# Optimization experiments

Hardware: AMD Instinct MI355X
Metric: run time of the kernel (lower is better)

Reference implementation:

```python
import jax, jax.numpy as jnp
import numpy as np

N = 50000      # nodes
E = 800000     # directed edges (before self-loops)
F_IN = 128     # input features
HID = 64       # hidden channels per head (conv1)
HEADS = 4      # attention heads (conv1)
C = 47         # num classes (conv2 out, 1 output head, concat=False)
NEG_SLOPE = 0.2


def _glorot(key, shape):
    fan = shape[0] + shape[-1] if len(shape) > 1 else shape[-1]
    lim = float(np.sqrt(6.0 / fan))
    return jax.random.uniform(key, shape, jnp.float32, -lim, lim)


def setup_inputs() -> dict:
    key = jax.random.key(0)
    ks = jax.random.split(key, 10)
    x = jax.random.normal(ks[0], (N, F_IN), jnp.float32)
    edge_index = jax.random.randint(ks[1], (2, E), 0, N, jnp.int32)
    W1 = _glorot(ks[2], (F_IN, HEADS * HID))
    a_src1 = _glorot(ks[3], (HEADS, HID))
    a_dst1 = _glorot(ks[4], (HEADS, HID))
    b1 = jnp.zeros((HEADS * HID,), jnp.float32)
    W2 = _glorot(ks[5], (HEADS * HID, 1 * C))
    a_src2 = _glorot(ks[6], (1, C))
    a_dst2 = _glorot(ks[7], (1, C))
    b2 = jnp.zeros((C,), jnp.float32)
    return {"x": x, "edge_index": edge_index, "W1": W1, "a_src1": a_src1,
            "a_dst1": a_dst1, "b1": b1, "W2": W2, "a_src2": a_src2,
            "a_dst2": a_dst2, "b2": b2}


def _gat_conv(x, W, a_src, a_dst, b, src, dst, n, heads, out_ch, concat):
    # linear transform, split heads: [n, heads, out_ch]
    h = (x @ W).reshape(n, heads, out_ch)
    # per-node attention logits
    al_s = jnp.sum(h * a_src, axis=-1)            # [n, heads]
    al_d = jnp.sum(h * a_dst, axis=-1)            # [n, heads]
    # per-edge scores (messages flow src -> dst)
    e = jax.nn.leaky_relu(al_s[src] + al_d[dst], NEG_SLOPE)  # [E', heads]
    # scatter-softmax over edges sharing a destination node
    e_max = jax.ops.segment_max(e, dst, num_segments=n)      # [n, heads]
    ex = jnp.exp(e - e_max[dst])
    denom = jax.ops.segment_sum(ex, dst, num_segments=n)
    alpha = ex / (denom[dst] + 1e-16)                        # [E', heads]
    # attention-weighted scatter-add aggregation
    out = jax.ops.segment_sum(h[src] * alpha[:, :, None], dst, num_segments=n)
    out = out.reshape(n, heads * out_ch) if concat else jnp.mean(out, axis=1)
    return out + b


def reference(x, edge_index, W1, a_src1, a_dst1, b1, W2, a_src2, a_dst2, b2):
    n = x.shape[0]
    # add self-loops (PyG GATConv default)
    loops = jnp.arange(n, dtype=edge_index.dtype)
    src = jnp.concatenate([edge_index[0], loops])
    dst = jnp.concatenate([edge_index[1], loops])
    # dropout omitted (eval mode)
    h = jax.nn.elu(_gat_conv(x, W1, a_src1, a_dst1, b1, src, dst, n, HEADS, HID, True))
    out = _gat_conv(h, W2, a_src2, a_dst2, b2, src, dst, n, 1, C, False)
    return jax.nn.log_softmax(out, axis=1)
```

## Files before the change

### kernel.cpp

```cpp
#include <hip/hip_runtime.h>
#include <hip/hip_fp16.h>
#include <math.h>

#define N_NODES 50000
#define E_EDGES 800000
#define E_TOT   850000
#define F_IN    128
#define C1      256
#define NCLS    47
#define H2S     48
#define NEG     0.2f
#define SCAN_B  196

typedef _Float16 f16x8 __attribute__((ext_vector_type(8)));
typedef float    f32x4 __attribute__((ext_vector_type(4)));


__global__ void k_count(const int* __restrict__ ei, int* __restrict__ deg) {
    int i = blockIdx.x * 256 + threadIdx.x;
    if (i >= E_TOT) return;
    int dst = (i < E_EDGES) ? ei[E_EDGES + i] : (i - E_EDGES);
    atomicAdd(&deg[dst], 1);
}

__global__ void k_scan_blk(const int* __restrict__ deg, int* __restrict__ blksum) {
    __shared__ int ws[4];
    int i = blockIdx.x * 256 + threadIdx.x;
    int v = (i < N_NODES) ? deg[i] : 0;
    int lane = threadIdx.x & 63, w = threadIdx.x >> 6;
    #pragma unroll
    for (int off = 32; off; off >>= 1) v += __shfl_xor(v, off);
    if (lane == 0) ws[w] = v;
    __syncthreads();
    if (threadIdx.x == 0) blksum[blockIdx.x] = ws[0] + ws[1] + ws[2] + ws[3];
}

__global__ void k_scan_top(const int* __restrict__ blksum, int* __restrict__ blkoff) {
    __shared__ int ws[4];
    int tid = threadIdx.x, lane = tid & 63, w = tid >> 6;
    int v = (tid < SCAN_B) ? blksum[tid] : 0;
    int sc = v;
    #pragma unroll
    for (int off = 1; off < 64; off <<= 1) {
        int t = __shfl_up(sc, off);
        if (lane >= off) sc += t;
    }
    if (lane == 63) ws[w] = sc;
    __syncthreads();
    if (tid == 0) { int a = 0; for (int t = 0; t < 4; t++) { int u = ws[t]; ws[t] = a; a += u; } }
    __syncthreads();
    if (tid < SCAN_B) blkoff[tid] = sc + ws[w] - v;
}

__global__ void k_scan_fin(const int* __restrict__ deg, const int* __restrict__ blkoff,
                           int* __restrict__ row_ptr, int* __restrict__ cursor) {
    __shared__ int ws[4];
    int i = blockIdx.x * 256 + threadIdx.x;
    int v = (i < N_NODES) ? deg[i] : 0;
    int lane = threadIdx.x & 63, w = threadIdx.x >> 6;
    int sc = v;
    #pragma unroll
    for (int off = 1; off < 64; off <<= 1) {
        int t = __shfl_up(sc, off);
        if (lane >= off) sc += t;
    }
    if (lane == 63) ws[w] = sc;
    __syncthreads();
    if (threadIdx.x == 0) { int a = 0; for (int t = 0; t < 4; t++) { int u = ws[t]; ws[t] = a; a += u; } }
    __syncthreads();
    int incl = sc + ws[w] + blkoff[blockIdx.x];
    if (i < N_NODES) {
        row_ptr[i + 1] = incl;
        cursor[i]      = incl - v;
    }
    if (i == 0) row_ptr[0] = 0;
}

__global__ void k_scatter(const int* __restrict__ ei, int* __restrict__ cursor,
                          int* __restrict__ csr_src) {
    int i = blockIdx.x * 256 + threadIdx.x;
    if (i >= E_TOT) return;
    int src, dst;
    if (i < E_EDGES) { src = ei[i]; dst = ei[E_EDGES + i]; }
    else             { src = dst = i - E_EDGES; }
    int pos = atomicAdd(&cursor[dst], 1);
    csr_src[pos] = src;
}


__global__ void k_prepw2f(const float* __restrict__ W2, uint4* __restrict__ W2f) {
    int t = blockIdx.x * 256 + threadIdx.x;
    if (t >= 1536) return;
    int f = t >> 9, ks = (t >> 6) & 7, lane = t & 63;
    int c  = f * 16 + (lane & 15);
    int kb = ks * 32 + ((lane >> 4) << 3);
    unsigned short h[8];
    #pragma unroll
    for (int j = 0; j < 8; j++) {
        float v = (c < NCLS) ? W2[(size_t)(kb + j) * NCLS + c] : 0.f;
        h[j] = __half_as_ushort(__float2half_rn(v));
    }
    W2f[t] = make_uint4((unsigned)h[0] | ((unsigned)h[1] << 16),
                        (unsigned)h[2] | ((unsigned)h[3] << 16),
                        (unsigned)h[4] | ((unsigned)h[5] << 16),
                        (unsigned)h[6] | ((unsigned)h[7] << 16));
}


__global__ void __launch_bounds__(64)
k_gemm1(const float* __restrict__ x, const float* __restrict__ W1,
        const float* __restrict__ a_src1, const float* __restrict__ a_dst1,
        __half* __restrict__ H1h, float* __restrict__ al_s, float* __restrict__ al_d) {
    __shared__ float xs[16][F_IN];
    int n0 = blockIdx.x * 16;
    int lane = threadIdx.x;
    {
        const float4* xg = (const float4*)(x + (size_t)n0 * F_IN);
        float4* xs4 = (float4*)&xs[0][0];
        #pragma unroll
        for (int j = 0; j < 8; j++) xs4[lane + 64 * j] = xg[lane + 64 * j];
    }
    __syncthreads();
    int c4 = lane * 4;
    float acc[16][4] = {};
    for (int kg = 0; kg < F_IN; kg += 4) {
        float4 w0 = *(const float4*)(W1 + (size_t)(kg + 0) * C1 + c4);
        float4 w1 = *(const float4*)(W1 + (size_t)(kg + 1) * C1 + c4);
        float4 w2 = *(const float4*)(W1 + (size_t)(kg + 2) * C1 + c4);
        float4 w3 = *(const float4*)(W1 + (size_t)(kg + 3) * C1 + c4);
        #pragma unroll
        for (int r = 0; r < 16; r++) {
            float4 xv = *(const float4*)&xs[r][kg];
            acc[r][0] += xv.x * w0.x + xv.y * w1.x + xv.z * w2.x + xv.w * w3.x;
            acc[r][1] += xv.x * w0.y + xv.y * w1.y + xv.z * w2.y + xv.w * w3.y;
            acc[r][2] += xv.x * w0.z + xv.y * w1.z + xv.z * w2.z + xv.w * w3.z;
            acc[r][3] += xv.x * w0.w + xv.y * w1.w + xv.z * w2.w + xv.w * w3.w;
        }
    }
    int h = lane >> 4;
    int cc4 = (lane & 15) * 4;
    float4 as = *(const float4*)(a_src1 + h * 64 + cc4);
    float4 ad = *(const float4*)(a_dst1 + h * 64 + cc4);
    #pragma unroll
    for (int r = 0; r < 16; r++) {
        int n = n0 + r;
        ushort4 pk;
        pk.x = __half_as_ushort(__float2half_rn(acc[r][0]));
        pk.y = __half_as_ushort(__float2half_rn(acc[r][1]));
        pk.z = __half_as_ushort(__float2half_rn(acc[r][2]));
        pk.w = __half_as_ushort(__float2half_rn(acc[r][3]));
        *(ushort4*)(H1h + (size_t)n * C1 + c4) = pk;
        float vs = acc[r][0]*as.x + acc[r][1]*as.y + acc[r][2]*as.z + acc[r][3]*as.w;
        float vd = acc[r][0]*ad.x + acc[r][1]*ad.y + acc[r][2]*ad.z + acc[r][3]*ad.w;
        #pragma unroll
        for (int off = 8; off; off >>= 1) {
            vs += __shfl_xor(vs, off);
            vd += __shfl_xor(vd, off);
        }
        if ((lane & 15) == 0) {
            al_s[n * 4 + h] = vs;
            al_d[n * 4 + h] = vd;
        }
    }
}


__global__ void k_agg1(const __half* __restrict__ H1h, const float* __restrict__ al_s,
                       const float* __restrict__ al_d, const int* __restrict__ row_ptr,
                       const int* __restrict__ csr_src, const float* __restrict__ b1,
                       __half* __restrict__ HEh) {
    int n = blockIdx.x * 4 + (threadIdx.x >> 6);
    int lane = threadIdx.x & 63;
    int h = lane >> 4;
    int beg = row_ptr[n], end = row_ptr[n + 1];
    float ald = al_d[n * 4 + h];
    float m = -INFINITY, s = 0.f;
    float a0 = 0.f, a1 = 0.f, a2 = 0.f, a3 = 0.f;
    int j = beg;
    for (; j + 3 < end; j += 4) {
        int ss[4]; float ee[4]; ushort4 hh[4];
        #pragma unroll
        for (int t = 0; t < 4; t++) ss[t] = csr_src[j + t];
        #pragma unroll
        for (int t = 0; t < 4; t++) ee[t] = al_s[ss[t] * 4 + h];
        #pragma unroll
        for (int t = 0; t < 4; t++)
            hh[t] = *(const ushort4*)(H1h + (size_t)ss[t] * C1 + lane * 4);
        #pragma unroll
        for (int t = 0; t < 4; t++) {
            float e = ee[t] + ald;
            ee[t] = (e >= 0.f) ? e : NEG * e;
        }
        float nm = fmaxf(m, fmaxf(fmaxf(ee[0], ee[1]), fmaxf(ee[2], ee[3])));
        float f = __expf(m - nm);
        m = nm;
        float p[4];
        #pragma unroll
        for (int t = 0; t < 4; t++) p[t] = __expf(ee[t] - nm);
        s = s * f + p[0] + p[1] + p[2] + p[3];
        a0 *= f; a1 *= f; a2 *= f; a3 *= f;
        #pragma unroll
        for (int t = 0; t < 4; t++) {
            a0 += p[t] * __half2float(__ushort_as_half(hh[t].x));
            a1 += p[t] * __half2float(__ushort_as_half(hh[t].y));
            a2 += p[t] * __half2float(__ushort_as_half(hh[t].z));
            a3 += p[t] * __half2float(__ushort_as_half(hh[t].w));
        }
    }
    for (; j < end; j++) {
        int s0 = csr_src[j];
        float e = al_s[s0 * 4 + h] + ald;
        e = (e >= 0.f) ? e : NEG * e;
        ushort4 hv = *(const ushort4*)(H1h + (size_t)s0 * C1 + lane * 4);
        float nm = fmaxf(m, e);
        float f  = __expf(m - nm);
        float pr = __expf(e - nm);
        s  = s  * f + pr;
        a0 = a0 * f + pr * __half2float(__ushort_as_half(hv.x));
        a1 = a1 * f + pr * __half2float(__ushort_as_half(hv.y));
        a2 = a2 * f + pr * __half2float(__ushort_as_half(hv.z));
        a3 = a3 * f + pr * __half2float(__ushort_as_half(hv.w));
        m = nm;
    }
    float inv = 1.f / (s + 1e-16f);
    float4 bb = *(const float4*)(b1 + lane * 4);
    float o0 = a0 * inv + bb.x, o1 = a1 * inv + bb.y;
    float o2 = a2 * inv + bb.z, o3 = a3 * inv + bb.w;
    o0 = (o0 > 0.f) ? o0 : expm1f(o0);
    o1 = (o1 > 0.f) ? o1 : expm1f(o1);
    o2 = (o2 > 0.f) ? o2 : expm1f(o2);
    o3 = (o3 > 0.f) ? o3 : expm1f(o3);
    ushort4 pk;
    pk.x = __half_as_ushort(__float2half_rn(o0));
    pk.y = __half_as_ushort(__float2half_rn(o1));
    pk.z = __half_as_ushort(__float2half_rn(o2));
    pk.w = __half_as_ushort(__float2half_rn(o3));
    *(ushort4*)(HEh + (size_t)n * C1 + lane * 4) = pk;
}


__global__ void __launch_bounds__(64)
k_gemm2(const __half* __restrict__ HEh, const uint4* __restrict__ W2f,
        const float* __restrict__ a_src2, const float* __restrict__ a_dst2,
        __half* __restrict__ H2h, float* __restrict__ al_s2, float* __restrict__ al_d2) {
    int lane = threadIdx.x;
    int n0 = blockIdx.x * 16;
    const __half* aptr = HEh + (size_t)(n0 + (lane & 15)) * C1 + ((lane >> 4) << 3);
    const f16x8* bptr = (const f16x8*)W2f;
    f32x4 acc0 = {0.f, 0.f, 0.f, 0.f};
    f32x4 acc1 = {0.f, 0.f, 0.f, 0.f};
    f32x4 acc2 = {0.f, 0.f, 0.f, 0.f};
    #pragma unroll
    for (int ks = 0; ks < 8; ks++) {
        f16x8 a  = *(const f16x8*)(aptr + ks * 32);
        f16x8 b0 = bptr[(0 * 8 + ks) * 64 + lane];
        f16x8 b1 = bptr[(1 * 8 + ks) * 64 + lane];
        f16x8 b2 = bptr[(2 * 8 + ks) * 64 + lane];
        acc0 = __builtin_amdgcn_mfma_f32_16x16x32_f16(a, b0, acc0, 0, 0, 0);
        acc1 = __builtin_amdgcn_mfma_f32_16x16x32_f16(a, b1, acc1, 0, 0, 0);
        acc2 = __builtin_amdgcn_mfma_f32_16x16x32_f16(a, b2, acc2, 0, 0, 0);
    }
    int col = lane & 15;
    int g4  = (lane >> 4) * 4;
    float as[3], ad[3];
    #pragma unroll
    for (int f = 0; f < 3; f++) {
        int c = f * 16 + col;
        as[f] = (c < NCLS) ? a_src2[c] : 0.f;
        ad[f] = (c < NCLS) ? a_dst2[c] : 0.f;
    }
    #pragma unroll
    for (int reg = 0; reg < 4; reg++) {
        int n = n0 + g4 + reg;
        float v0 = acc0[reg], v1 = acc1[reg], v2 = acc2[reg];
        __half* orow = H2h + (size_t)n * H2S;
        orow[col]      = __float2half_rn(v0);
        orow[16 + col] = __float2half_rn(v1);
        orow[32 + col] = __float2half_rn(v2);
        float vs = v0 * as[0] + v1 * as[1] + v2 * as[2];
        float vd = v0 * ad[0] + v1 * ad[1] + v2 * ad[2];
        #pragma unroll
        for (int off = 8; off; off >>= 1) {
            vs += __shfl_xor(vs, off);
            vd += __shfl_xor(vd, off);
        }
        if (col == 0) { al_s2[n] = vs; al_d2[n] = vd; }
    }
}


__global__ void k_agg2(const __half* __restrict__ H2h, const float* __restrict__ al_s2,
                       const float* __restrict__ al_d2, const int* __restrict__ row_ptr,
                       const int* __restrict__ csr_src, const float* __restrict__ b2,
                       float* __restrict__ out) {
    int n = blockIdx.x * 4 + (threadIdx.x >> 6);
    if (n >= N_NODES) return;
    int lane = threadIdx.x & 63;
    int beg = row_ptr[n], end = row_ptr[n + 1];
    float ald = al_d2[n];
    float m = -INFINITY, s = 0.f, acc = 0.f;
    int j = beg;
    for (; j + 3 < end; j += 4) {
        int ss[4]; float ee[4]; float hv[4];
        #pragma unroll
        for (int t = 0; t < 4; t++) ss[t] = csr_src[j + t];
        #pragma unroll
        for (int t = 0; t < 4; t++) ee[t] = al_s2[ss[t]];
        #pragma unroll
        for (int t = 0; t < 4; t++)
            hv[t] = (lane < NCLS) ? __half2float(H2h[(size_t)ss[t] * H2S + lane]) : 0.f;
        #pragma unroll
        for (int t = 0; t < 4; t++) {
            float e = ee[t] + ald;
            ee[t] = (e >= 0.f) ? e : NEG * e;
        }
        float nm = fmaxf(m, fmaxf(fmaxf(ee[0], ee[1]), fmaxf(ee[2], ee[3])));
        float f = __expf(m - nm);
        m = nm;
        float p[4];
        #pragma unroll
        for (int t = 0; t < 4; t++) p[t] = __expf(ee[t] - nm);
        s = s * f + p[0] + p[1] + p[2] + p[3];
        acc = acc * f + p[0] * hv[0] + p[1] * hv[1] + p[2] * hv[2] + p[3] * hv[3];
    }
    for (; j < end; j++) {
        int src = csr_src[j];
        float e = al_s2[src] + ald;
        e = (e >= 0.f) ? e : NEG * e;
        float hv = (lane < NCLS) ? __half2float(H2h[(size_t)src * H2S + lane]) : 0.f;
        float nm = fmaxf(m, e);
        float f  = __expf(m - nm);
        float pr = __expf(e - nm);
        s   = s   * f + pr;
        acc = acc * f + pr * hv;
        m = nm;
    }
    float v = acc / (s + 1e-16f) + ((lane < NCLS) ? b2[lane] : -INFINITY);
    float mx = v;
    #pragma unroll
    for (int off = 32; off; off >>= 1) mx = fmaxf(mx, __shfl_xor(mx, off));
    float ex = __expf(v - mx);
    float sum = ex;
    #pragma unroll
    for (int off = 32; off; off >>= 1) sum += __shfl_xor(sum, off);
    if (lane < NCLS) out[(size_t)n * NCLS + lane] = v - mx - logf(sum);
}


extern "C" void kernel_launch(void* const* d_in, const int* in_sizes, int n_in,
                              void* d_out, int out_size, void* d_ws, size_t ws_size,
                              hipStream_t stream) {
    const float* x      = (const float*)d_in[0];
    const int*   ei     = (const int*)  d_in[1];
    const float* W1     = (const float*)d_in[2];
    const float* a_src1 = (const float*)d_in[3];
    const float* a_dst1 = (const float*)d_in[4];
    const float* b1     = (const float*)d_in[5];
    const float* W2     = (const float*)d_in[6];
    const float* a_src2 = (const float*)d_in[7];
    const float* a_dst2 = (const float*)d_in[8];
    const float* b2     = (const float*)d_in[9];
    float* out = (float*)d_out;

    char* base = (char*)d_ws;
    size_t off = 0;
    auto alloc = [&](size_t bytes) -> void* {
        void* r = base + off;
        off += (bytes + 511) & ~size_t(511);
        return r;
    };
    __half* H1h   = (__half*)alloc((size_t)N_NODES * C1 * 2);
    __half* HEh   = (__half*)alloc((size_t)N_NODES * C1 * 2);
    __half* H2h   = (__half*)alloc((size_t)N_NODES * H2S * 2);
    uint4*  W2f   = (uint4*) alloc((size_t)1536 * 16);
    float*  al_s1 = (float*) alloc((size_t)N_NODES * 4 * 4);
    float*  al_d1 = (float*) alloc((size_t)N_NODES * 4 * 4);
    float*  al_s2 = (float*) alloc((size_t)N_NODES * 4);
    float*  al_d2 = (float*) alloc((size_t)N_NODES * 4);
    int*    deg   = (int*)   alloc((size_t)N_NODES * 4);
    int*    rowp  = (int*)   alloc((size_t)(N_NODES + 1) * 4);
    int*    cursor= (int*)   alloc((size_t)N_NODES * 4);
    int*    blks  = (int*)   alloc((size_t)SCAN_B * 4);
    int*    blko  = (int*)   alloc((size_t)SCAN_B * 4);
    int*    csrs  = (int*)   alloc((size_t)E_TOT * 4);

    hipMemsetAsync(deg, 0, (size_t)N_NODES * 4, stream);

    int eb = (E_TOT + 255) / 256;
    k_count   <<<eb, 256, 0, stream>>>(ei, deg);
    k_scan_blk<<<SCAN_B, 256, 0, stream>>>(deg, blks);
    k_scan_top<<<1, 256, 0, stream>>>(blks, blko);
    k_scan_fin<<<SCAN_B, 256, 0, stream>>>(deg, blko, rowp, cursor);
    k_scatter <<<eb, 256, 0, stream>>>(ei, cursor, csrs);
    k_prepw2f <<<6, 256, 0, stream>>>(W2, W2f);

    k_gemm1<<<N_NODES / 16, 64, 0, stream>>>(x, W1, a_src1, a_dst1, H1h, al_s1, al_d1);
    k_agg1 <<<(N_NODES + 3) / 4, 256, 0, stream>>>(H1h, al_s1, al_d1, rowp, csrs, b1, HEh);
    k_gemm2<<<N_NODES / 16, 64, 0, stream>>>(HEh, W2f, a_src2, a_dst2, H2h, al_s2, al_d2);
    k_agg2 <<<(N_NODES + 3) / 4, 256, 0, stream>>>(H2h, al_s2, al_d2, rowp, csrs, b2, out);
}
```

Before: 390.8 us.

## Move first GAT linear layer to fp16 MFMA with pre-packed weights

Replaces the fp32 FMA-based x@W1 kernel with one that uses the 16x16x32 fp16 MFMA instruction. It adds a pass that converts x to half precision and another that packs W1 into the MFMA operand layout, mirroring the existing W2 path. The attention logits are now reduced from the MFMA accumulator layout. The cost is an extra read and write of x for the conversion, fp16 rounding of the inputs, and H1 stores that are now scalar halves instead of packed ushort4.

```diff
diff --git a/kernel.cpp b/kernel.cpp
--- a/kernel.cpp
+++ b/kernel.cpp
@@ -88,6 +88,36 @@
 }
 
 
+__global__ void k_prepx(const float* __restrict__ x, __half* __restrict__ xh) {
+    int i = blockIdx.x * 256 + threadIdx.x;
+    if (i >= N_NODES * F_IN / 4) return;
+    float4 v = ((const float4*)x)[i];
+    ushort4 p;
+    p.x = __half_as_ushort(__float2half_rn(v.x));
+    p.y = __half_as_ushort(__float2half_rn(v.y));
+    p.z = __half_as_ushort(__float2half_rn(v.z));
+    p.w = __half_as_ushort(__float2half_rn(v.w));
+    ((ushort4*)xh)[i] = p;
+}
+
+
+__global__ void k_prepw1f(const float* __restrict__ W1, uint4* __restrict__ W1f) {
+    int t = blockIdx.x * 256 + threadIdx.x;
+    if (t >= 4096) return;
+    int f = t >> 8, ks = (t >> 6) & 3, lane = t & 63;
+    int c  = f * 16 + (lane & 15);
+    int kb = ks * 32 + ((lane >> 4) << 3);
+    unsigned short h[8];
+    #pragma unroll
+    for (int j = 0; j < 8; j++)
+        h[j] = __half_as_ushort(__float2half_rn(W1[(size_t)(kb + j) * C1 + c]));
+    W1f[t] = make_uint4((unsigned)h[0] | ((unsigned)h[1] << 16),
+                        (unsigned)h[2] | ((unsigned)h[3] << 16),
+                        (unsigned)h[4] | ((unsigned)h[5] << 16),
+                        (unsigned)h[6] | ((unsigned)h[7] << 16));
+}
+
+
 __global__ void k_prepw2f(const float* __restrict__ W2, uint4* __restrict__ W2f) {
     int t = blockIdx.x * 256 + threadIdx.x;
     if (t >= 1536) return;
@@ -108,58 +138,59 @@
 
 
 __global__ void __launch_bounds__(64)
-k_gemm1(const float* __restrict__ x, const float* __restrict__ W1,
+k_gemm1(const __half* __restrict__ xh, const uint4* __restrict__ W1f,
         const float* __restrict__ a_src1, const float* __restrict__ a_dst1,
         __half* __restrict__ H1h, float* __restrict__ al_s, float* __restrict__ al_d) {
-    __shared__ float xs[16][F_IN];
+    int lane = threadIdx.x;
     int n0 = blockIdx.x * 16;
-    int lane = threadIdx.x;
-    {
-        const float4* xg = (const float4*)(x + (size_t)n0 * F_IN);
-        float4* xs4 = (float4*)&xs[0][0];
-        #pragma unroll
-        for (int j = 0; j < 8; j++) xs4[lane + 64 * j] = xg[lane + 64 * j];
-    }
-    __syncthreads();
-    int c4 = lane * 4;
-    float acc[16][4] = {};
-    for (int kg = 0; kg < F_IN; kg += 4) {
-        float4 w0 = *(const float4*)(W1 + (size_t)(kg + 0) * C1 + c4);
-        float4 w1 = *(const float4*)(W1 + (size_t)(kg + 1) * C1 + c4);
-        float4 w2 = *(const float4*)(W1 + (size_t)(kg + 2) * C1 + c4);
-        float4 w3 = *(const float4*)(W1 + (size_t)(kg + 3) * C1 + c4);
-        #pragma unroll
-        for (int r = 0; r < 16; r++) {
-            float4 xv = *(const float4*)&xs[r][kg];
-            acc[r][0] += xv.x * w0.x + xv.y * w1.x + xv.z * w2.x + xv.w * w3.x;
-            acc[r][1] += xv.x * w0.y + xv.y * w1.y + xv.z * w2.y + xv.w * w3.y;
-            acc[r][2] += xv.x * w0.z + xv.y * w1.z + xv.z * w2.z + xv.w * w3.z;
-            acc[r][3] += xv.x * w0.w + xv.y * w1.w + xv.z * w2.w + xv.w * w3.w;
-        }
-    }
-    int h = lane >> 4;
-    int cc4 = (lane & 15) * 4;
-    float4 as = *(const float4*)(a_src1 + h * 64 + cc4);
-    float4 ad = *(const float4*)(a_dst1 + h * 64 + cc4);
-    #pragma unroll
-    for (int r = 0; r < 16; r++) {
-        int n = n0 + r;
-        ushort4 pk;
-        pk.x = __half_as_ushort(__float2half_rn(acc[r][0]));
-        pk.y = __half_as_ushort(__float2half_rn(acc[r][1]));
-        pk.z = __half_as_ushort(__float2half_rn(acc[r][2]));
-        pk.w = __half_as_ushort(__float2half_rn(acc[r][3]));
-        *(ushort4*)(H1h + (size_t)n * C1 + c4) = pk;
-        float vs = acc[r][0]*as.x + acc[r][1]*as.y + acc[r][2]*as.z + acc[r][3]*as.w;
-        float vd = acc[r][0]*ad.x + acc[r][1]*ad.y + acc[r][2]*ad.z + acc[r][3]*ad.w;
-        #pragma unroll
-        for (int off = 8; off; off >>= 1) {
-            vs += __shfl_xor(vs, off);
-            vd += __shfl_xor(vd, off);
-        }
-        if ((lane & 15) == 0) {
-            al_s[n * 4 + h] = vs;
-            al_d[n * 4 + h] = vd;
+    const __half* aptr = xh + (size_t)(n0 + (lane & 15)) * F_IN + ((lane >> 4) << 3);
+    const f16x8* bptr = (const f16x8*)W1f;
+    f32x4 acc[16];
+    #pragma unroll
+    for (int f = 0; f < 16; f++) acc[f] = (f32x4){0.f, 0.f, 0.f, 0.f};
+    #pragma unroll
+    for (int ks = 0; ks < 4; ks++) {
+        f16x8 a = *(const f16x8*)(aptr + ks * 32);
+        #pragma unroll
+        for (int f = 0; f < 16; f++) {
+            f16x8 b = bptr[(f * 4 + ks) * 64 + lane];
+            acc[f] = __builtin_amdgcn_mfma_f32_16x16x32_f16(a, b, acc[f], 0, 0, 0);
+        }
+    }
+    int col = lane & 15;
+    int g4  = (lane >> 4) * 4;
+    float asf[16], adf[16];
+    #pragma unroll
+    for (int f = 0; f < 16; f++) {
+        asf[f] = a_src1[f * 16 + col];
+        adf[f] = a_dst1[f * 16 + col];
+    }
+    #pragma unroll
+    for (int reg = 0; reg < 4; reg++) {
+        int n = n0 + g4 + reg;
+        float vs[4] = {0.f, 0.f, 0.f, 0.f};
+        float vd[4] = {0.f, 0.f, 0.f, 0.f};
+        #pragma unroll
+        for (int f = 0; f < 16; f++) {
+            float v = acc[f][reg];
+            H1h[(size_t)n * C1 + f * 16 + col] = __float2half_rn(v);
+            vs[f >> 2] += v * asf[f];
+            vd[f >> 2] += v * adf[f];
+        }
+        #pragma unroll
+        for (int h = 0; h < 4; h++) {
+            #pragma unroll
+            for (int off = 8; off; off >>= 1) {
+                vs[h] += __shfl_xor(vs[h], off);
+                vd[h] += __shfl_xor(vd[h], off);
+            }
+        }
+        if (col == 0) {
+            #pragma unroll
+            for (int h = 0; h < 4; h++) {
+                al_s[n * 4 + h] = vs[h];
+                al_d[n * 4 + h] = vd[h];
+            }
         }
     }
 }
@@ -372,6 +403,8 @@
     __half* H1h   = (__half*)alloc((size_t)N_NODES * C1 * 2);
     __half* HEh   = (__half*)alloc((size_t)N_NODES * C1 * 2);
     __half* H2h   = (__half*)alloc((size_t)N_NODES * H2S * 2);
+    __half* xh    = (__half*)alloc((size_t)N_NODES * F_IN * 2);
+    uint4*  W1f   = (uint4*) alloc((size_t)4096 * 16);
     uint4*  W2f   = (uint4*) alloc((size_t)1536 * 16);
     float*  al_s1 = (float*) alloc((size_t)N_NODES * 4 * 4);
     float*  al_d1 = (float*) alloc((size_t)N_NODES * 4 * 4);
@@ -392,9 +425,11 @@
     k_scan_top<<<1, 256, 0, stream>>>(blks, blko);
     k_scan_fin<<<SCAN_B, 256, 0, stream>>>(deg, blko, rowp, cursor);
     k_scatter <<<eb, 256, 0, stream>>>(ei, cursor, csrs);
+    k_prepx   <<<(N_NODES * F_IN / 4 + 255) / 256, 256, 0, stream>>>(x, xh);
+    k_prepw1f <<<16, 256, 0, stream>>>(W1, W1f);
     k_prepw2f <<<6, 256, 0, stream>>>(W2, W2f);
 
-    k_gemm1<<<N_NODES / 16, 64, 0, stream>>>(x, W1, a_src1, a_dst1, H1h, al_s1, al_d1);
+    k_gemm1<<<N_NODES / 16, 64, 0, stream>>>(xh, W1f, a_src1, a_dst1, H1h, al_s1, al_d1);
     k_agg1 <<<(N_NODES + 3) / 4, 256, 0, stream>>>(H1h, al_s1, al_d1, rowp, csrs, b1, HEh);
     k_gemm2<<<N_NODES / 16, 64, 0, stream>>>(HEh, W2f, a_src2, a_dst2, H2h, al_s2, al_d2);
     k_agg2 <<<(N_NODES + 3) / 4, 256, 0, stream>>>(H2h, al_s2, al_d2, rowp, csrs, b2, out);
```

After: 349.1 us. 10.7% less time.
